# Optimization experiments

Measured on AMD Instinct MI355X. Metric: run time of the kernel, lower is better.

The kernel has to match this reference:

```python
import jax, jax.numpy as jnp
import numpy as np

NUM_USERS = 50000
NUM_ITEMS = 50000
EMB_K = 8
N = 8192
GAMMA = 0.1


def setup_inputs() -> dict:
    key = jax.random.key(0)
    ks = jax.random.split(key, 11)
    s = 1.0
    return {
        "x": jax.random.randint(ks[0], (N, 2), 0, NUM_ITEMS, dtype=jnp.int64) if jax.config.jax_enable_x64 else jax.random.randint(ks[0], (N, 2), 0, NUM_ITEMS),
        "y": jax.random.randint(ks[1], (N, 2), 0, NUM_ITEMS),
        "W": jax.random.normal(ks[2], (NUM_USERS, EMB_K), jnp.float32) * s,
        "H": jax.random.normal(ks[3], (NUM_ITEMS, EMB_K), jnp.float32) * s,
        "ncf_user_emb": jax.random.normal(ks[4], (NUM_USERS, EMB_K), jnp.float32) * s,
        "ncf_item_emb": jax.random.normal(ks[5], (NUM_ITEMS, EMB_K), jnp.float32) * s,
        "lin1_w": jax.random.normal(ks[6], (EMB_K, 2 * EMB_K), jnp.float32) * 0.1,
        "lin1_b": jax.random.normal(ks[7], (EMB_K,), jnp.float32) * 0.1,
        "lin2_w": jax.random.normal(ks[8], (1, EMB_K), jnp.float32) * 0.1,
        "mf_user_emb": jax.random.normal(ks[9], (NUM_USERS, EMB_K), jnp.float32) * s,
        "mf_item_emb": jax.random.normal(ks[10], (NUM_ITEMS, EMB_K), jnp.float32) * s,
    }


def _get_embedding(idx, Wt, Ht):
    # concat user/item embeddings -> [N, 2k], then the (buggy, faithful) min/max step
    feat = jnp.concatenate([Wt[idx[:, 0]], Ht[idx[:, 1]]], axis=1)
    f_min = jnp.min(feat)
    f_max = jnp.max(feat)
    feat = feat - f_min / (f_max - f_min)  # scalar division binds first, as in source
    return feat / feat.shape[1]


def _exp_kernel(X, Y, gamma):
    # Euclidean cdist(Y, X) via gram trick (no [Ny,Nx,d] intermediate), then exp(-d*gamma)
    d2 = (jnp.sum(Y * Y, axis=1)[:, None]
          + jnp.sum(X * X, axis=1)[None, :]
          - 2.0 * (Y @ X.T))
    d = jnp.sqrt(jnp.maximum(d2, 0.0))
    return jnp.exp(-d * gamma)


def reference(x, y, W, H, ncf_user_emb, ncf_item_emb, lin1_w, lin1_b, lin2_w, mf_user_emb, mf_item_emb):
    # kernel branch
    fx = _get_embedding(x, W, H)  # [N, 2k]
    fy = _get_embedding(y, W, H)  # [N, 2k]
    K = _exp_kernel(fx, fy, GAMMA)  # [Ny, Nx]
    # NCF prediction model on x
    ue = ncf_user_emb[x[:, 0]]
    ie = ncf_item_emb[x[:, 1]]
    z = jnp.concatenate([ue, ie], axis=1)
    h1 = jax.nn.relu(z @ lin1_w.T + lin1_b)
    pred = h1 @ lin2_w.T  # [N, 1]
    # MF weight model on x
    mu = mf_user_emb[x[:, 0]]
    mi = mf_item_emb[x[:, 1]]
    w = jnp.sum(mu * mi, axis=1, keepdims=True)  # [N, 1]
    return (K, pred, w)
```

## Files before the change

kernel.cpp:

```cpp
#include <hip/hip_runtime.h>

#define NN 8192
#define GAMMA 0.1f

typedef float v2f __attribute__((ext_vector_type(2)));
typedef float v4f __attribute__((ext_vector_type(4)));

__global__ __launch_bounds__(256) void prep_kernel(
    const int* __restrict__ x, const int* __restrict__ y,
    const float* __restrict__ W, const float* __restrict__ H,
    const float* __restrict__ nue, const float* __restrict__ nie,
    const float* __restrict__ l1w, const float* __restrict__ l1b,
    const float* __restrict__ l2w,
    const float* __restrict__ mfu, const float* __restrict__ mfi,
    float* __restrict__ pred, float* __restrict__ wout,
    float* __restrict__ pmn, float* __restrict__ pmx)
{
    int gid = blockIdx.x * 256 + threadIdx.x;
    bool isx = gid < NN;
    int i = isx ? gid : gid - NN;
    const int* idx = isx ? x : y;
    int iu = idx[2 * i], iv = idx[2 * i + 1];

    const float4* wp = (const float4*)(W + (size_t)iu * 8);
    float4 w0 = wp[0], w1 = wp[1];
    const float4* hp = (const float4*)(H + (size_t)iv * 8);
    float4 h0 = hp[0], h1 = hp[1];

    float f[16];
    f[0] = w0.x; f[1] = w0.y; f[2] = w0.z; f[3] = w0.w;
    f[4] = w1.x; f[5] = w1.y; f[6] = w1.z; f[7] = w1.w;
    f[8] = h0.x; f[9] = h0.y; f[10] = h0.z; f[11] = h0.w;
    f[12] = h1.x; f[13] = h1.y; f[14] = h1.z; f[15] = h1.w;

    float mn = f[0], mx = f[0];
#pragma unroll
    for (int k = 1; k < 16; k++) { mn = fminf(mn, f[k]); mx = fmaxf(mx, f[k]); }
#pragma unroll
    for (int off = 1; off < 64; off <<= 1) {
        mn = fminf(mn, __shfl_xor(mn, off));
        mx = fmaxf(mx, __shfl_xor(mx, off));
    }
    if ((threadIdx.x & 63) == 0) {
        int wid = gid >> 6;
        pmn[wid] = mn;
        pmx[wid] = mx;
    }

    if (isx) {
        const float4* up = (const float4*)(nue + (size_t)iu * 8);
        float4 u0 = up[0], u1 = up[1];
        const float4* ip = (const float4*)(nie + (size_t)iv * 8);
        float4 i0 = ip[0], i1 = ip[1];
        float z[16];
        z[0] = u0.x; z[1] = u0.y; z[2] = u0.z; z[3] = u0.w;
        z[4] = u1.x; z[5] = u1.y; z[6] = u1.z; z[7] = u1.w;
        z[8] = i0.x; z[9] = i0.y; z[10] = i0.z; z[11] = i0.w;
        z[12] = i1.x; z[13] = i1.y; z[14] = i1.z; z[15] = i1.w;

        float p = 0.f;
#pragma unroll
        for (int k = 0; k < 8; k++) {
            float h = l1b[k];
#pragma unroll
            for (int m = 0; m < 16; m++) h = fmaf(z[m], l1w[k * 16 + m], h);
            h = fmaxf(h, 0.f);
            p = fmaf(h, l2w[k], p);
        }
        pred[i] = p;

        const float4* ap = (const float4*)(mfu + (size_t)iu * 8);
        float4 a0 = ap[0], a1 = ap[1];
        const float4* bp = (const float4*)(mfi + (size_t)iv * 8);
        float4 b0 = bp[0], b1 = bp[1];
        float wv = a0.x * b0.x + a0.y * b0.y + a0.z * b0.z + a0.w * b0.w
                 + a1.x * b1.x + a1.y * b1.y + a1.z * b1.z + a1.w * b1.w;
        wout[i] = wv;
    }
}

__global__ __launch_bounds__(256) void norm_kernel(
    const int* __restrict__ x, const int* __restrict__ y,
    const float* __restrict__ W, const float* __restrict__ H,
    const float* __restrict__ pmn, const float* __restrict__ pmx,
    float* __restrict__ fxs, float* __restrict__ fyn,
    float* __restrict__ nx, float* __restrict__ ny)
{
    __shared__ float red[256];
    int tid = threadIdx.x;
    int gid = blockIdx.x * 256 + tid;
    bool isx = gid < NN;
    int side = isx ? 0 : 1;

    if (tid < 128) red[tid] = pmn[side * 128 + tid];
    else           red[tid] = pmx[side * 128 + (tid - 128)];
    __syncthreads();
#pragma unroll
    for (int s = 64; s >= 1; s >>= 1) {
        if ((tid & 127) < s) {
            float o = red[tid + s];
            red[tid] = (tid < 128) ? fminf(red[tid], o) : fmaxf(red[tid], o);
        }
        __syncthreads();
    }
    float fmn = red[0], fmx = red[128];
    float c = fmn / (fmx - fmn);

    int i = isx ? gid : gid - NN;
    const int* idx = isx ? x : y;
    int iu = idx[2 * i], iv = idx[2 * i + 1];
    const float4* wp = (const float4*)(W + (size_t)iu * 8);
    float4 w0 = wp[0], w1 = wp[1];
    const float4* hp = (const float4*)(H + (size_t)iv * 8);
    float4 h0 = hp[0], h1 = hp[1];

    float f[16];
    f[0] = w0.x; f[1] = w0.y; f[2] = w0.z; f[3] = w0.w;
    f[4] = w1.x; f[5] = w1.y; f[6] = w1.z; f[7] = w1.w;
    f[8] = h0.x; f[9] = h0.y; f[10] = h0.z; f[11] = h0.w;
    f[12] = h1.x; f[13] = h1.y; f[14] = h1.z; f[15] = h1.w;

    float g[16];
    float s = 0.f;
    float sc2 = isx ? -2.f : 1.f;
    float o[16];
#pragma unroll
    for (int k = 0; k < 16; k++) {
        g[k] = (f[k] - c) * (1.f / 16.f);
        s = fmaf(g[k], g[k], s);
        o[k] = g[k] * sc2;
    }
    float* dst = (isx ? fxs : fyn) + (size_t)i * 16;
    float4* dv = (float4*)dst;
    dv[0] = make_float4(o[0], o[1], o[2], o[3]);
    dv[1] = make_float4(o[4], o[5], o[6], o[7]);
    dv[2] = make_float4(o[8], o[9], o[10], o[11]);
    dv[3] = make_float4(o[12], o[13], o[14], o[15]);
    (isx ? nx : ny)[i] = s;
}

__global__ __launch_bounds__(256) void kexp_kernel(
    const float* __restrict__ fxs, const float* __restrict__ fyn,
    const float* __restrict__ nx, const float* __restrict__ ny,
    float* __restrict__ K)
{
    __shared__ float sfy[512];
    __shared__ float sny[32];
    int tid = threadIdx.x;
    int ib = blockIdx.y * 32;
    int jb = blockIdx.x * 1024;

    for (int t = tid; t < 512; t += 256) sfy[t] = fyn[(size_t)ib * 16 + t];
    if (tid < 32) sny[tid] = ny[ib + tid];
    __syncthreads();

    int j0 = jb + tid * 4;
    v2f a[4][8];
    float nxr[4];
#pragma unroll
    for (int c2 = 0; c2 < 4; c2++) {
        const float4* p = (const float4*)(fxs + (size_t)(j0 + c2) * 16);
        float4 v0 = p[0], v1 = p[1], v2 = p[2], v3 = p[3];
        a[c2][0] = (v2f){v0.x, v0.y}; a[c2][1] = (v2f){v0.z, v0.w};
        a[c2][2] = (v2f){v1.x, v1.y}; a[c2][3] = (v2f){v1.z, v1.w};
        a[c2][4] = (v2f){v2.x, v2.y}; a[c2][5] = (v2f){v2.z, v2.w};
        a[c2][6] = (v2f){v3.x, v3.y}; a[c2][7] = (v2f){v3.z, v3.w};
        nxr[c2] = nx[j0 + c2];
    }

    const float4* sfy4 = (const float4*)sfy;
    const float CC = 2.0813689894397856e-2f;

#pragma unroll 2
    for (int i = 0; i < 32; i++) {
        float4 q0 = sfy4[i * 4 + 0], q1 = sfy4[i * 4 + 1];
        float4 q2 = sfy4[i * 4 + 2], q3 = sfy4[i * 4 + 3];
        v2f fy[8];
        fy[0] = (v2f){q0.x, q0.y}; fy[1] = (v2f){q0.z, q0.w};
        fy[2] = (v2f){q1.x, q1.y}; fy[3] = (v2f){q1.z, q1.w};
        fy[4] = (v2f){q2.x, q2.y}; fy[5] = (v2f){q2.z, q2.w};
        fy[6] = (v2f){q3.x, q3.y}; fy[7] = (v2f){q3.z, q3.w};
        float nyv = sny[i];
        float r[4];
#pragma unroll
        for (int c2 = 0; c2 < 4; c2++) {
            v2f acc = (v2f){nyv + nxr[c2], 0.f};
#pragma unroll
            for (int k = 0; k < 8; k++)
                acc = __builtin_elementwise_fma(a[c2][k], fy[k], acc);
            float d2 = fmaxf(acc.x + acc.y, 0.f);
            r[c2] = __builtin_amdgcn_exp2f(-__builtin_amdgcn_sqrtf(d2 * CC));
        }
        v4f o = (v4f){r[0], r[1], r[2], r[3]};
        __builtin_nontemporal_store(o, (v4f*)(K + (size_t)(ib + i) * NN + j0));
    }
}

extern "C" void kernel_launch(void* const* d_in, const int* in_sizes, int n_in,
                              void* d_out, int out_size, void* d_ws, size_t ws_size,
                              hipStream_t stream) {
    const int* x = (const int*)d_in[0];
    const int* y = (const int*)d_in[1];
    const float* W = (const float*)d_in[2];
    const float* H = (const float*)d_in[3];
    const float* nue = (const float*)d_in[4];
    const float* nie = (const float*)d_in[5];
    const float* l1w = (const float*)d_in[6];
    const float* l1b = (const float*)d_in[7];
    const float* l2w = (const float*)d_in[8];
    const float* mfu = (const float*)d_in[9];
    const float* mfi = (const float*)d_in[10];

    float* out = (float*)d_out;
    float* K = out;
    float* pred = out + (size_t)NN * NN;
    float* wout = pred + NN;

    float* pmn = (float*)d_ws;
    float* pmx = pmn + 256;
    float* fxs = pmx + 256;
    float* fyn = fxs + (size_t)NN * 16;
    float* nx  = fyn + (size_t)NN * 16;
    float* ny  = nx + NN;

    hipLaunchKernelGGL(prep_kernel, dim3(64), dim3(256), 0, stream,
                       x, y, W, H, nue, nie, l1w, l1b, l2w, mfu, mfi, pred, wout, pmn, pmx);
    hipLaunchKernelGGL(norm_kernel, dim3(64), dim3(256), 0, stream,
                       x, y, W, H, pmn, pmx, fxs, fyn, nx, ny);
    hipLaunchKernelGGL(kexp_kernel, dim3(8, 256), dim3(256), 0, stream,
                       fxs, fyn, nx, ny, K);
}
```

Measured before the change: 60.24 us.

## Shrink prep/norm blocks, shuffle-reduce min/max, fold scale constant, drop LDS staging

Prep and norm kernels now use smaller blocks (64 and 128 threads), so more workgroups are spread across CUs. The norm kernel replaces the shared-memory tree reduction with a wave-shuffle reduction. The exp-kernel scale constant is folded into the y features and norms, which removes one multiply per output element. The kexp kernel no longer stages fy rows in LDS and instead reads them straight from global memory, which removes a barrier but relies on caches serving the row loads that all threads repeat.

```diff
diff --git a/kernel.cpp b/kernel.cpp
--- a/kernel.cpp
+++ b/kernel.cpp
@@ -6,7 +6,7 @@
 typedef float v2f __attribute__((ext_vector_type(2)));
 typedef float v4f __attribute__((ext_vector_type(4)));
 
-__global__ __launch_bounds__(256) void prep_kernel(
+__global__ __launch_bounds__(64) void prep_kernel(
     const int* __restrict__ x, const int* __restrict__ y,
     const float* __restrict__ W, const float* __restrict__ H,
     const float* __restrict__ nue, const float* __restrict__ nie,
@@ -16,7 +16,7 @@
     float* __restrict__ pred, float* __restrict__ wout,
     float* __restrict__ pmn, float* __restrict__ pmx)
 {
-    int gid = blockIdx.x * 256 + threadIdx.x;
+    int gid = blockIdx.x * 64 + threadIdx.x;
     bool isx = gid < NN;
     int i = isx ? gid : gid - NN;
     const int* idx = isx ? x : y;
@@ -41,10 +41,9 @@
         mn = fminf(mn, __shfl_xor(mn, off));
         mx = fmaxf(mx, __shfl_xor(mx, off));
     }
-    if ((threadIdx.x & 63) == 0) {
-        int wid = gid >> 6;
-        pmn[wid] = mn;
-        pmx[wid] = mx;
+    if (threadIdx.x == 0) {
+        pmn[blockIdx.x] = mn;
+        pmx[blockIdx.x] = mx;
     }
 
     if (isx) {
@@ -79,31 +78,35 @@
     }
 }
 
-__global__ __launch_bounds__(256) void norm_kernel(
+__global__ __launch_bounds__(128) void norm_kernel(
     const int* __restrict__ x, const int* __restrict__ y,
     const float* __restrict__ W, const float* __restrict__ H,
     const float* __restrict__ pmn, const float* __restrict__ pmx,
     float* __restrict__ fxs, float* __restrict__ fyn,
     float* __restrict__ nx, float* __restrict__ ny)
 {
-    __shared__ float red[256];
+    __shared__ float sred[2];
     int tid = threadIdx.x;
-    int gid = blockIdx.x * 256 + tid;
+    int gid = blockIdx.x * 128 + tid;
     bool isx = gid < NN;
     int side = isx ? 0 : 1;
-
-    if (tid < 128) red[tid] = pmn[side * 128 + tid];
-    else           red[tid] = pmx[side * 128 + (tid - 128)];
+    const float CC = 2.0813689894397856e-2f;
+
+    {
+        int ln = tid & 63;
+        bool ismax = tid >= 64;
+        const float* psrc = ismax ? pmx : pmn;
+        float u0 = psrc[side * 128 + ln], u1 = psrc[side * 128 + ln + 64];
+        float v = ismax ? fmaxf(u0, u1) : fminf(u0, u1);
+#pragma unroll
+        for (int off = 1; off < 64; off <<= 1) {
+            float o = __shfl_xor(v, off);
+            v = ismax ? fmaxf(v, o) : fminf(v, o);
+        }
+        if (ln == 0) sred[ismax ? 1 : 0] = v;
+    }
     __syncthreads();
-#pragma unroll
-    for (int s = 64; s >= 1; s >>= 1) {
-        if ((tid & 127) < s) {
-            float o = red[tid + s];
-            red[tid] = (tid < 128) ? fminf(red[tid], o) : fmaxf(red[tid], o);
-        }
-        __syncthreads();
-    }
-    float fmn = red[0], fmx = red[128];
+    float fmn = sred[0], fmx = sred[1];
     float c = fmn / (fmx - fmn);
 
     int i = isx ? gid : gid - NN;
@@ -120,10 +123,9 @@
     f[8] = h0.x; f[9] = h0.y; f[10] = h0.z; f[11] = h0.w;
     f[12] = h1.x; f[13] = h1.y; f[14] = h1.z; f[15] = h1.w;
 
-    float g[16];
+    float g[16], o[16];
     float s = 0.f;
-    float sc2 = isx ? -2.f : 1.f;
-    float o[16];
+    float sc2 = isx ? -2.f : CC;
 #pragma unroll
     for (int k = 0; k < 16; k++) {
         g[k] = (f[k] - c) * (1.f / 16.f);
@@ -136,7 +138,7 @@
     dv[1] = make_float4(o[4], o[5], o[6], o[7]);
     dv[2] = make_float4(o[8], o[9], o[10], o[11]);
     dv[3] = make_float4(o[12], o[13], o[14], o[15]);
-    (isx ? nx : ny)[i] = s;
+    (isx ? nx : ny)[i] = s * CC;
 }
 
 __global__ __launch_bounds__(256) void kexp_kernel(
@@ -144,15 +146,9 @@
     const float* __restrict__ nx, const float* __restrict__ ny,
     float* __restrict__ K)
 {
-    __shared__ float sfy[512];
-    __shared__ float sny[32];
     int tid = threadIdx.x;
     int ib = blockIdx.y * 32;
     int jb = blockIdx.x * 1024;
-
-    for (int t = tid; t < 512; t += 256) sfy[t] = fyn[(size_t)ib * 16 + t];
-    if (tid < 32) sny[tid] = ny[ib + tid];
-    __syncthreads();
 
     int j0 = jb + tid * 4;
     v2f a[4][8];
@@ -168,19 +164,16 @@
         nxr[c2] = nx[j0 + c2];
     }
 
-    const float4* sfy4 = (const float4*)sfy;
-    const float CC = 2.0813689894397856e-2f;
-
 #pragma unroll 2
     for (int i = 0; i < 32; i++) {
-        float4 q0 = sfy4[i * 4 + 0], q1 = sfy4[i * 4 + 1];
-        float4 q2 = sfy4[i * 4 + 2], q3 = sfy4[i * 4 + 3];
+        const float4* fq = (const float4*)(fyn + (size_t)(ib + i) * 16);
+        float4 q0 = fq[0], q1 = fq[1], q2 = fq[2], q3 = fq[3];
+        float nyv = ny[ib + i];
         v2f fy[8];
         fy[0] = (v2f){q0.x, q0.y}; fy[1] = (v2f){q0.z, q0.w};
         fy[2] = (v2f){q1.x, q1.y}; fy[3] = (v2f){q1.z, q1.w};
         fy[4] = (v2f){q2.x, q2.y}; fy[5] = (v2f){q2.z, q2.w};
         fy[6] = (v2f){q3.x, q3.y}; fy[7] = (v2f){q3.z, q3.w};
-        float nyv = sny[i];
         float r[4];
 #pragma unroll
         for (int c2 = 0; c2 < 4; c2++) {
@@ -189,7 +182,7 @@
             for (int k = 0; k < 8; k++)
                 acc = __builtin_elementwise_fma(a[c2][k], fy[k], acc);
             float d2 = fmaxf(acc.x + acc.y, 0.f);
-            r[c2] = __builtin_amdgcn_exp2f(-__builtin_amdgcn_sqrtf(d2 * CC));
+            r[c2] = __builtin_amdgcn_exp2f(-__builtin_amdgcn_sqrtf(d2));
         }
         v4f o = (v4f){r[0], r[1], r[2], r[3]};
         __builtin_nontemporal_store(o, (v4f*)(K + (size_t)(ib + i) * NN + j0));
@@ -223,9 +216,9 @@
     float* nx  = fyn + (size_t)NN * 16;
     float* ny  = nx + NN;
 
-    hipLaunchKernelGGL(prep_kernel, dim3(64), dim3(256), 0, stream,
+    hipLaunchKernelGGL(prep_kernel, dim3(256), dim3(64), 0, stream,
                        x, y, W, H, nue, nie, l1w, l1b, l2w, mfu, mfi, pred, wout, pmn, pmx);
-    hipLaunchKernelGGL(norm_kernel, dim3(64), dim3(256), 0, stream,
+    hipLaunchKernelGGL(norm_kernel, dim3(128), dim3(128), 0, stream,
                        x, y, W, H, pmn, pmx, fxs, fyn, nx, ny);
     hipLaunchKernelGGL(kexp_kernel, dim3(8, 256), dim3(256), 0, stream,
                        fxs, fyn, nx, ny, K);
```

Result: slower. 67.15 us (+11.5%).
